# Optimization experiments

Measured on AMD Instinct MI355X. Metric: run time of the kernel, lower is better.

The kernel has to match this reference:

```python
import jax, jax.numpy as jnp
import numpy as np

D_MODEL = 1024
N_HEAD = 16
HEAD_DIM = D_MODEL // N_HEAD


def setup_inputs() -> dict:
    key = jax.random.key(0)
    k1, k2, k3 = jax.random.split(key, 3)
    x = jax.random.normal(k1, (2, 2048, D_MODEL), dtype=jnp.float32)
    w_qkv = jax.random.normal(k2, (D_MODEL, 3 * D_MODEL), dtype=jnp.float32) * (1.0 / np.sqrt(D_MODEL))
    w_proj = jax.random.normal(k3, (D_MODEL, D_MODEL), dtype=jnp.float32) * (1.0 / np.sqrt(D_MODEL))
    return {"x": x, "w_qkv": w_qkv, "w_proj": w_proj}


def reference(x, w_qkv, w_proj):
    bs, sl, dm = x.shape
    qkv = x @ w_qkv                                   # [B,S,3*D]
    qkv = qkv.reshape(bs, sl, 3, N_HEAD, HEAD_DIM)
    q, k, v = qkv[:, :, 0], qkv[:, :, 1], qkv[:, :, 2]  # [B,S,H,d]
    q = q.transpose(0, 2, 1, 3)                        # [B,H,S,d]
    k = k.transpose(0, 2, 1, 3)
    v = v.transpose(0, 2, 1, 3)
    sc = 1.0 / np.sqrt(HEAD_DIM).astype(np.float32)
    attn = jnp.einsum('bhqd,bhkd->bhqk', q, k) * sc    # [B,H,S,S]
    causal = jnp.tril(jnp.ones((sl, sl), dtype=bool))  # True = keep
    attn = jnp.where(causal, attn, -jnp.inf)
    w = jax.nn.softmax(attn, axis=-1)                  # [B,H,S,S] (dropout p=0)
    o = jnp.einsum('bhqk,bhkd->bhqd', w, v)            # [B,H,S,d]
    out = o.transpose(0, 2, 1, 3).reshape(bs, sl, dm)
    out = out @ w_proj
    return (out, w)
```

## Files before the change

kernel.cpp:

```cpp
#include <hip/hip_runtime.h>

typedef _Float16 half8 __attribute__((ext_vector_type(8)));
typedef _Float16 half4 __attribute__((ext_vector_type(4)));
typedef float f32x4 __attribute__((ext_vector_type(4)));

__device__ __forceinline__ void gl2lds16(const _Float16* g, _Float16* l) {
  __builtin_amdgcn_global_load_lds((const __attribute__((address_space(1))) void*)g,
                                   (__attribute__((address_space(3))) void*)l, 16, 0, 0);
}

__device__ __forceinline__ void nt_store4(float* p, f32x4 v) {
  __builtin_nontemporal_store(v, (f32x4*)p);
}

__global__ __launch_bounds__(256) void cvt_kernel(const float* __restrict__ in,
                                                  _Float16* __restrict__ out, int n) {
  int i = (blockIdx.x * 256 + threadIdx.x) * 8;
  if (i >= n) return;
  float4 a = *(const float4*)(in + i);
  float4 b = *(const float4*)(in + i + 4);
  half8 o;
  o[0] = (_Float16)a.x; o[1] = (_Float16)a.y; o[2] = (_Float16)a.z; o[3] = (_Float16)a.w;
  o[4] = (_Float16)b.x; o[5] = (_Float16)b.y; o[6] = (_Float16)b.z; o[7] = (_Float16)b.w;
  *(half8*)(out + i) = o;
}

__global__ __launch_bounds__(256) void cvtT_kernel(const float* __restrict__ in,
                                                   _Float16* __restrict__ out,
                                                   int K, int N) {
  __shared__ float Ts[64][65];
  const int k0 = blockIdx.y * 64, n0 = blockIdx.x * 64;
  const int t = threadIdx.x;
  const int r = t >> 4, c = (t & 15) * 4;
#pragma unroll
  for (int i = 0; i < 4; i++) {
    float4 v = *(const float4*)(in + (size_t)(k0 + r + i * 16) * N + n0 + c);
    Ts[r + i * 16][c] = v.x; Ts[r + i * 16][c + 1] = v.y;
    Ts[r + i * 16][c + 2] = v.z; Ts[r + i * 16][c + 3] = v.w;
  }
  __syncthreads();
  const int nl = t >> 2, kq = (t & 3) * 16;
  half8 o0, o1;
#pragma unroll
  for (int j = 0; j < 8; j++) {
    o0[j] = (_Float16)Ts[kq + j][nl];
    o1[j] = (_Float16)Ts[kq + 8 + j][nl];
  }
  *(half8*)(out + (size_t)(n0 + nl) * K + k0 + kq) = o0;
  *(half8*)(out + (size_t)(n0 + nl) * K + k0 + kq + 8) = o1;
}

__global__ __launch_bounds__(256) void vtrans_kernel(const _Float16* __restrict__ v,
                                                     _Float16* __restrict__ vt) {
  __shared__ _Float16 Ht[64][72];
  const int s0 = blockIdx.x * 64;
  const _Float16* vb = v + (size_t)blockIdx.y * 131072;
  _Float16* vtb = vt + (size_t)blockIdx.y * 131072;
  const int t = threadIdx.x;
  const int sl = t >> 3, dq = (t & 7) * 8;
  *(half8*)&Ht[sl][dq] = *(const half8*)(vb + (s0 + sl) * 64 + dq);
  *(half8*)&Ht[sl + 32][dq] = *(const half8*)(vb + (s0 + sl + 32) * 64 + dq);
  __syncthreads();
  const int dl = t >> 2, sq = (t & 3) * 16;
  half8 o0, o1;
#pragma unroll
  for (int j = 0; j < 8; j++) {
    o0[j] = Ht[sq + j][dl];
    o1[j] = Ht[sq + 8 + j][dl];
  }
  *(half8*)(vtb + (size_t)dl * 2048 + s0 + sq) = o0;
  *(half8*)(vtb + (size_t)dl * 2048 + s0 + sq + 8) = o1;
}

template <int MODE, int BN>
__global__ __launch_bounds__(256) void gemm16(const _Float16* __restrict__ A,
                                              const _Float16* __restrict__ B,
                                              float* __restrict__ Cf,
                                              _Float16* __restrict__ Ch,
                                              int M, int N, int K) {
  constexpr int MI = (BN == 128) ? 4 : 2;
  __shared__ __align__(16) _Float16 As[128 * 32];
  __shared__ __align__(16) _Float16 Bs[BN * 32];
  const int tid = threadIdx.x;
  const int lane = tid & 63;
  const int wid = tid >> 6;
  const int quad = lane >> 4;
  const int l16 = lane & 15;
  const int mbase = (BN == 128) ? (wid >> 1) * 64 : wid * 32;
  const int nbase = (BN == 128) ? (wid & 1) * 64 : 0;
  const int m0 = blockIdx.y * 128;
  const int n0 = blockIdx.x * BN;

  f32x4 acc[MI][4];
  const f32x4 fz = {0.f, 0.f, 0.f, 0.f};
#pragma unroll
  for (int i = 0; i < MI; i++)
#pragma unroll
    for (int j = 0; j < 4; j++) acc[i][j] = fz;

  const int srow = tid >> 2;
  const int kq = (tid & 3) * 8;

  for (int kt = 0; kt < K; kt += 32) {
    gl2lds16(A + (size_t)(m0 + srow) * K + kt + kq, &As[tid * 8]);
    gl2lds16(A + (size_t)(m0 + 64 + srow) * K + kt + kq, &As[2048 + tid * 8]);
    gl2lds16(B + (size_t)(n0 + srow) * K + kt + kq, &Bs[tid * 8]);
    if (BN == 128)
      gl2lds16(B + (size_t)(n0 + 64 + srow) * K + kt + kq, &Bs[2048 + tid * 8]);
    __syncthreads();
    half8 af[MI], bf[4];
#pragma unroll
    for (int mi = 0; mi < MI; mi++)
      af[mi] = *(const half8*)&As[(mbase + mi * 16 + l16) * 32 + quad * 8];
#pragma unroll
    for (int ni = 0; ni < 4; ni++)
      bf[ni] = *(const half8*)&Bs[(nbase + ni * 16 + l16) * 32 + quad * 8];
#pragma unroll
    for (int mi = 0; mi < MI; mi++)
#pragma unroll
      for (int ni = 0; ni < 4; ni++)
        acc[mi][ni] = __builtin_amdgcn_mfma_f32_16x16x32_f16(af[mi], bf[ni], acc[mi][ni], 0, 0, 0);
    __syncthreads();
  }

#pragma unroll
  for (int mi = 0; mi < MI; mi++)
#pragma unroll
    for (int ni = 0; ni < 4; ni++)
#pragma unroll
      for (int r = 0; r < 4; r++) {
        int row = m0 + mbase + mi * 16 + quad * 4 + r;
        int col = n0 + nbase + ni * 16 + l16;
        float v = acc[mi][ni][r];
        if (MODE == 0) {
          Cf[(size_t)row * N + col] = v;
        } else {
          int which = col >> 10, h = (col >> 6) & 15, d = col & 63;
          int b = row >> 11, s = row & 2047;
          Ch[((((size_t)(which * 2 + b) * 16 + h) * 2048) + s) * 64 + d] = (_Float16)v;
        }
      }
}

__global__ __launch_bounds__(256) void attn_kernel(const _Float16* __restrict__ qkv,
                                                   const _Float16* __restrict__ vt,
                                                   float* __restrict__ w_out,
                                                   _Float16* __restrict__ o_buf) {
  const int qt = 31 - blockIdx.x;
  const int bh = blockIdx.y;
  const int tid = threadIdx.x;
  const int lane = tid & 63;
  const int wid = tid >> 6;
  const int quad = lane >> 4;
  const int l16 = lane & 15;

  const _Float16* qp = qkv + (size_t)bh * 131072;
  const _Float16* kp = qp + 4194304;
  const _Float16* vtb = vt + (size_t)bh * 131072;

  __shared__ __align__(16) _Float16 Ks[2][4096];
  __shared__ __align__(16) _Float16 Vs[2][4096];
  __shared__ __align__(16) _Float16 Ps[64][72];

  const int qrow = qt * 64 + wid * 16 + l16;
  const half8 qa0 = *(const half8*)(qp + qrow * 64 + quad * 8);
  const half8 qa1 = *(const half8*)(qp + qrow * 64 + 32 + quad * 8);

  const int srow = tid >> 2;
  const int blk8 = (tid & 3) * 8;
  const float sc = 0.125f;
  const f32x4 fz = {0.f, 0.f, 0.f, 0.f};
  const int lrow0 = wid * 16 + quad * 4;

  float* wbase = w_out + (size_t)bh * 4194304 + (size_t)qt * 131072;

  {
    const int rr = tid >> 4, cc = (tid & 15) * 4;
    for (int kt = qt + 1; kt < 32; kt++) {
      float* wz = wbase + (size_t)kt * 64 + cc;
#pragma unroll
      for (int p = 0; p < 4; p++)
        nt_store4(wz + (size_t)(p * 16 + rr) * 2048, fz);
    }
  }

  float lsum[4] = {0.f, 0.f, 0.f, 0.f};

  int cur = 0;
  gl2lds16(kp + (size_t)srow * 64 + blk8, &Ks[0][tid * 8]);
  gl2lds16(kp + (size_t)srow * 64 + 32 + blk8, &Ks[0][2048 + tid * 8]);
  __syncthreads();
  for (int kt = 0; kt <= qt; kt++) {
    if (kt < qt) {
      gl2lds16(kp + (size_t)((kt + 1) * 64 + srow) * 64 + blk8, &Ks[cur ^ 1][tid * 8]);
      gl2lds16(kp + (size_t)((kt + 1) * 64 + srow) * 64 + 32 + blk8, &Ks[cur ^ 1][2048 + tid * 8]);
    }
    f32x4 sacc[4];
#pragma unroll
    for (int ni = 0; ni < 4; ni++) {
      half8 kb0 = *(const half8*)&Ks[cur][(ni * 16 + l16) * 32 + quad * 8];
      half8 kb1 = *(const half8*)&Ks[cur][2048 + (ni * 16 + l16) * 32 + quad * 8];
      f32x4 s = fz;
      s = __builtin_amdgcn_mfma_f32_16x16x32_f16(qa0, kb0, s, 0, 0, 0);
      s = __builtin_amdgcn_mfma_f32_16x16x32_f16(qa1, kb1, s, 0, 0, 0);
      sacc[ni] = s;
    }
    if (kt < qt) {
#pragma unroll
      for (int ni = 0; ni < 4; ni++)
#pragma unroll
        for (int r = 0; r < 4; r++) lsum[r] += __expf(sacc[ni][r] * sc);
    } else {
#pragma unroll
      for (int ni = 0; ni < 4; ni++)
#pragma unroll
        for (int r = 0; r < 4; r++) {
          if (ni * 16 + l16 <= lrow0 + r) lsum[r] += __expf(sacc[ni][r] * sc);
        }
    }
    __syncthreads();
    cur ^= 1;
  }
  float invl[4];
#pragma unroll
  for (int r = 0; r < 4; r++) {
    float s = lsum[r];
    s += __shfl_xor(s, 1); s += __shfl_xor(s, 2);
    s += __shfl_xor(s, 4); s += __shfl_xor(s, 8);
    invl[r] = 1.0f / s;
  }

  f32x4 oacc[4];
#pragma unroll
  for (int di = 0; di < 4; di++) oacc[di] = fz;

  cur = 0;
  gl2lds16(kp + (size_t)srow * 64 + blk8, &Ks[0][tid * 8]);
  gl2lds16(kp + (size_t)srow * 64 + 32 + blk8, &Ks[0][2048 + tid * 8]);
  gl2lds16(vtb + (size_t)srow * 2048 + blk8, &Vs[0][tid * 8]);
  gl2lds16(vtb + (size_t)srow * 2048 + 32 + blk8, &Vs[0][2048 + tid * 8]);
  __syncthreads();
  for (int kt = 0; kt <= qt; kt++) {
    if (kt < qt) {
      const int kn = kt + 1;
      gl2lds16(kp + (size_t)(kn * 64 + srow) * 64 + blk8, &Ks[cur ^ 1][tid * 8]);
      gl2lds16(kp + (size_t)(kn * 64 + srow) * 64 + 32 + blk8, &Ks[cur ^ 1][2048 + tid * 8]);
      gl2lds16(vtb + (size_t)srow * 2048 + kn * 64 + blk8, &Vs[cur ^ 1][tid * 8]);
      gl2lds16(vtb + (size_t)srow * 2048 + kn * 64 + 32 + blk8, &Vs[cur ^ 1][2048 + tid * 8]);
    }
    f32x4 sacc[4];
#pragma unroll
    for (int ni = 0; ni < 4; ni++) {
      half8 kb0 = *(const half8*)&Ks[cur][(ni * 16 + l16) * 32 + quad * 8];
      half8 kb1 = *(const half8*)&Ks[cur][2048 + (ni * 16 + l16) * 32 + quad * 8];
      f32x4 s = fz;
      s = __builtin_amdgcn_mfma_f32_16x16x32_f16(qa0, kb0, s, 0, 0, 0);
      s = __builtin_amdgcn_mfma_f32_16x16x32_f16(qa1, kb1, s, 0, 0, 0);
      sacc[ni] = s;
    }
#pragma unroll
    for (int ni = 0; ni < 4; ni++)
#pragma unroll
      for (int r = 0; r < 4; r++) {
        int lrw = lrow0 + r;
        int col = ni * 16 + l16;
        float p = __expf(sacc[ni][r] * sc) * invl[r];
        if (kt == qt && col > lrw) p = 0.0f;
        Ps[lrw][col] = (_Float16)p;
      }
#pragma unroll
    for (int kk = 0; kk < 2; kk++) {
      half8 pa = *(const half8*)&Ps[wid * 16 + l16][kk * 32 + quad * 8];
#pragma unroll
      for (int di = 0; di < 4; di++) {
        half8 vb = *(const half8*)&Vs[cur][kk * 2048 + (di * 16 + l16) * 32 + quad * 8];
        oacc[di] = __builtin_amdgcn_mfma_f32_16x16x32_f16(pa, vb, oacc[di], 0, 0, 0);
      }
    }
    {
      const int erow = lane >> 2;
      const int ec = (lane & 3) * 4;
      const _Float16* prow = &Ps[wid * 16 + erow][0];
      float* wrow = wbase + (size_t)(wid * 16 + erow) * 2048 + kt * 64;
#pragma unroll
      for (int j = 0; j < 4; j++) {
        half4 h = *(const half4*)(prow + j * 16 + ec);
        f32x4 o;
        o[0] = (float)h[0]; o[1] = (float)h[1]; o[2] = (float)h[2]; o[3] = (float)h[3];
        nt_store4(wrow + j * 16 + ec, o);
      }
    }
    __syncthreads();
    cur ^= 1;
  }

  const int b = bh >> 4, h = bh & 15;
#pragma unroll
  for (int di = 0; di < 4; di++)
#pragma unroll
    for (int r = 0; r < 4; r++) {
      int s = qt * 64 + lrow0 + r;
      int d = di * 16 + l16;
      o_buf[((size_t)(b * 2048 + s) * 16 + h) * 64 + d] = (_Float16)oacc[di][r];
    }
}

extern "C" void kernel_launch(void* const* d_in, const int* in_sizes, int n_in,
                              void* d_out, int out_size, void* d_ws, size_t ws_size,
                              hipStream_t stream) {
  const float* x = (const float*)d_in[0];
  const float* w_qkv = (const float*)d_in[1];
  const float* w_proj = (const float*)d_in[2];
  float* out = (float*)d_out;
  float* w_attn = out + (size_t)4194304;

  char* ws = (char*)d_ws;
  _Float16* x16 = (_Float16*)ws;
  _Float16* wqkvT = (_Float16*)(ws + (size_t)(8 << 20));
  _Float16* wprojT = (_Float16*)(ws + (size_t)(14 << 20));
  _Float16* qkvb = (_Float16*)(ws + (size_t)(16 << 20));
  _Float16* vT = (_Float16*)(ws + (size_t)(40 << 20));
  _Float16* ob = (_Float16*)(ws + (size_t)(48 << 20));

  cvt_kernel<<<2048, 256, 0, stream>>>(x, x16, 4194304);
  cvtT_kernel<<<dim3(48, 16), 256, 0, stream>>>(w_qkv, wqkvT, 1024, 3072);
  cvtT_kernel<<<dim3(16, 16), 256, 0, stream>>>(w_proj, wprojT, 1024, 1024);

  gemm16<1, 128><<<dim3(24, 32), 256, 0, stream>>>(x16, wqkvT, nullptr, qkvb, 4096, 3072, 1024);
  vtrans_kernel<<<dim3(32, 32), 256, 0, stream>>>(qkvb + (size_t)2 * 4194304, vT);
  attn_kernel<<<dim3(32, 32), 256, 0, stream>>>(qkvb, vT, w_attn, ob);
  gemm16<0, 64><<<dim3(16, 32), 256, 0, stream>>>(ob, wprojT, out, nullptr, 4096, 1024, 1024);
}
```

Before: 699.1 us.

## Load K/V fragments straight from global memory, drop LDS staging and barriers

The attention kernel stops staging K and V tiles through double-buffered LDS with global_load_lds and block-wide barriers. Each wave now reads its MFMA operand fragments directly from global memory and relies on the caches for reuse across waves. The softmax scale is folded into Q at the QKV GEMM epilogue, and s_setprio is raised around the MFMA sections. The aim is to remove barrier stalls and LDS traffic, at the cost of more global and L2 load requests and exposed load latency with no explicit prefetch.

```diff
diff --git a/kernel.cpp b/kernel.cpp
--- a/kernel.cpp
+++ b/kernel.cpp
@@ -137,6 +137,7 @@
         } else {
           int which = col >> 10, h = (col >> 6) & 15, d = col & 63;
           int b = row >> 11, s = row & 2047;
+          if (which == 0) v *= 0.125f;
           Ch[((((size_t)(which * 2 + b) * 16 + h) * 2048) + s) * 64 + d] = (_Float16)v;
         }
       }
@@ -158,17 +159,12 @@
   const _Float16* kp = qp + 4194304;
   const _Float16* vtb = vt + (size_t)bh * 131072;
 
-  __shared__ __align__(16) _Float16 Ks[2][4096];
-  __shared__ __align__(16) _Float16 Vs[2][4096];
   __shared__ __align__(16) _Float16 Ps[64][72];
 
   const int qrow = qt * 64 + wid * 16 + l16;
   const half8 qa0 = *(const half8*)(qp + qrow * 64 + quad * 8);
   const half8 qa1 = *(const half8*)(qp + qrow * 64 + 32 + quad * 8);
 
-  const int srow = tid >> 2;
-  const int blk8 = (tid & 3) * 8;
-  const float sc = 0.125f;
   const f32x4 fz = {0.f, 0.f, 0.f, 0.f};
   const int lrow0 = wid * 16 + quad * 4;
 
@@ -186,40 +182,33 @@
 
   float lsum[4] = {0.f, 0.f, 0.f, 0.f};
 
-  int cur = 0;
-  gl2lds16(kp + (size_t)srow * 64 + blk8, &Ks[0][tid * 8]);
-  gl2lds16(kp + (size_t)srow * 64 + 32 + blk8, &Ks[0][2048 + tid * 8]);
-  __syncthreads();
   for (int kt = 0; kt <= qt; kt++) {
-    if (kt < qt) {
-      gl2lds16(kp + (size_t)((kt + 1) * 64 + srow) * 64 + blk8, &Ks[cur ^ 1][tid * 8]);
-      gl2lds16(kp + (size_t)((kt + 1) * 64 + srow) * 64 + 32 + blk8, &Ks[cur ^ 1][2048 + tid * 8]);
-    }
+    const _Float16* kb = kp + (size_t)kt * 4096;
     f32x4 sacc[4];
+    __builtin_amdgcn_s_setprio(1);
 #pragma unroll
     for (int ni = 0; ni < 4; ni++) {
-      half8 kb0 = *(const half8*)&Ks[cur][(ni * 16 + l16) * 32 + quad * 8];
-      half8 kb1 = *(const half8*)&Ks[cur][2048 + (ni * 16 + l16) * 32 + quad * 8];
+      half8 kb0 = *(const half8*)(kb + (ni * 16 + l16) * 64 + quad * 8);
+      half8 kb1 = *(const half8*)(kb + (ni * 16 + l16) * 64 + 32 + quad * 8);
       f32x4 s = fz;
       s = __builtin_amdgcn_mfma_f32_16x16x32_f16(qa0, kb0, s, 0, 0, 0);
       s = __builtin_amdgcn_mfma_f32_16x16x32_f16(qa1, kb1, s, 0, 0, 0);
       sacc[ni] = s;
     }
+    __builtin_amdgcn_s_setprio(0);
     if (kt < qt) {
 #pragma unroll
       for (int ni = 0; ni < 4; ni++)
 #pragma unroll
-        for (int r = 0; r < 4; r++) lsum[r] += __expf(sacc[ni][r] * sc);
+        for (int r = 0; r < 4; r++) lsum[r] += __expf(sacc[ni][r]);
     } else {
 #pragma unroll
       for (int ni = 0; ni < 4; ni++)
 #pragma unroll
         for (int r = 0; r < 4; r++) {
-          if (ni * 16 + l16 <= lrow0 + r) lsum[r] += __expf(sacc[ni][r] * sc);
+          if (ni * 16 + l16 <= lrow0 + r) lsum[r] += __expf(sacc[ni][r]);
         }
     }
-    __syncthreads();
-    cur ^= 1;
   }
   float invl[4];
 #pragma unroll
@@ -234,49 +223,41 @@
 #pragma unroll
   for (int di = 0; di < 4; di++) oacc[di] = fz;
 
-  cur = 0;
-  gl2lds16(kp + (size_t)srow * 64 + blk8, &Ks[0][tid * 8]);
-  gl2lds16(kp + (size_t)srow * 64 + 32 + blk8, &Ks[0][2048 + tid * 8]);
-  gl2lds16(vtb + (size_t)srow * 2048 + blk8, &Vs[0][tid * 8]);
-  gl2lds16(vtb + (size_t)srow * 2048 + 32 + blk8, &Vs[0][2048 + tid * 8]);
-  __syncthreads();
   for (int kt = 0; kt <= qt; kt++) {
-    if (kt < qt) {
-      const int kn = kt + 1;
-      gl2lds16(kp + (size_t)(kn * 64 + srow) * 64 + blk8, &Ks[cur ^ 1][tid * 8]);
-      gl2lds16(kp + (size_t)(kn * 64 + srow) * 64 + 32 + blk8, &Ks[cur ^ 1][2048 + tid * 8]);
-      gl2lds16(vtb + (size_t)srow * 2048 + kn * 64 + blk8, &Vs[cur ^ 1][tid * 8]);
-      gl2lds16(vtb + (size_t)srow * 2048 + kn * 64 + 32 + blk8, &Vs[cur ^ 1][2048 + tid * 8]);
-    }
+    const _Float16* kb = kp + (size_t)kt * 4096;
     f32x4 sacc[4];
+    __builtin_amdgcn_s_setprio(1);
 #pragma unroll
     for (int ni = 0; ni < 4; ni++) {
-      half8 kb0 = *(const half8*)&Ks[cur][(ni * 16 + l16) * 32 + quad * 8];
-      half8 kb1 = *(const half8*)&Ks[cur][2048 + (ni * 16 + l16) * 32 + quad * 8];
+      half8 kb0 = *(const half8*)(kb + (ni * 16 + l16) * 64 + quad * 8);
+      half8 kb1 = *(const half8*)(kb + (ni * 16 + l16) * 64 + 32 + quad * 8);
       f32x4 s = fz;
       s = __builtin_amdgcn_mfma_f32_16x16x32_f16(qa0, kb0, s, 0, 0, 0);
       s = __builtin_amdgcn_mfma_f32_16x16x32_f16(qa1, kb1, s, 0, 0, 0);
       sacc[ni] = s;
     }
+    __builtin_amdgcn_s_setprio(0);
 #pragma unroll
     for (int ni = 0; ni < 4; ni++)
 #pragma unroll
       for (int r = 0; r < 4; r++) {
         int lrw = lrow0 + r;
         int col = ni * 16 + l16;
-        float p = __expf(sacc[ni][r] * sc) * invl[r];
+        float p = __expf(sacc[ni][r]) * invl[r];
         if (kt == qt && col > lrw) p = 0.0f;
         Ps[lrw][col] = (_Float16)p;
       }
+    __builtin_amdgcn_s_setprio(1);
 #pragma unroll
     for (int kk = 0; kk < 2; kk++) {
       half8 pa = *(const half8*)&Ps[wid * 16 + l16][kk * 32 + quad * 8];
 #pragma unroll
       for (int di = 0; di < 4; di++) {
-        half8 vb = *(const half8*)&Vs[cur][kk * 2048 + (di * 16 + l16) * 32 + quad * 8];
+        half8 vb = *(const half8*)(vtb + (size_t)(di * 16 + l16) * 2048 + kt * 64 + kk * 32 + quad * 8);
         oacc[di] = __builtin_amdgcn_mfma_f32_16x16x32_f16(pa, vb, oacc[di], 0, 0, 0);
       }
     }
+    __builtin_amdgcn_s_setprio(0);
     {
       const int erow = lane >> 2;
       const int ec = (lane & 3) * 4;
@@ -290,8 +271,6 @@
         nt_store4(wrow + j * 16 + ec, o);
       }
     }
-    __syncthreads();
-    cur ^= 1;
   }
 
   const int b = bh >> 4, h = bh & 15;
```

Result: slower. 889.4 us (+27.2%).

## Fold softmax scale into Q and load V fragments directly from global

Applied to the files above, without the earlier changes.

The QKV GEMM epilogue now multiplies Q by 1/sqrt(d) before storing it, so the attention kernel no longer scales each score before the exponential. The V tile is no longer staged through double-buffered shared memory with global-to-LDS copies. Each wave instead loads its V MFMA fragments straight from global memory into registers at the start of each key tile. The barrier is moved to sit before the W store. This cuts LDS traffic and footprint and drops one multiply per score, but each wave now loads V redundantly, and that load latency is hidden only behind the QK MFMAs.

```diff
diff --git a/kernel.cpp b/kernel.cpp
--- a/kernel.cpp
+++ b/kernel.cpp
@@ -137,6 +137,7 @@
         } else {
           int which = col >> 10, h = (col >> 6) & 15, d = col & 63;
           int b = row >> 11, s = row & 2047;
+          if (which == 0) v *= 0.125f;
           Ch[((((size_t)(which * 2 + b) * 16 + h) * 2048) + s) * 64 + d] = (_Float16)v;
         }
       }
@@ -159,7 +160,6 @@
   const _Float16* vtb = vt + (size_t)bh * 131072;
 
   __shared__ __align__(16) _Float16 Ks[2][4096];
-  __shared__ __align__(16) _Float16 Vs[2][4096];
   __shared__ __align__(16) _Float16 Ps[64][72];
 
   const int qrow = qt * 64 + wid * 16 + l16;
@@ -168,7 +168,6 @@
 
   const int srow = tid >> 2;
   const int blk8 = (tid & 3) * 8;
-  const float sc = 0.125f;
   const f32x4 fz = {0.f, 0.f, 0.f, 0.f};
   const int lrow0 = wid * 16 + quad * 4;
 
@@ -209,13 +208,13 @@
 #pragma unroll
       for (int ni = 0; ni < 4; ni++)
 #pragma unroll
-        for (int r = 0; r < 4; r++) lsum[r] += __expf(sacc[ni][r] * sc);
+        for (int r = 0; r < 4; r++) lsum[r] += __expf(sacc[ni][r]);
     } else {
 #pragma unroll
       for (int ni = 0; ni < 4; ni++)
 #pragma unroll
         for (int r = 0; r < 4; r++) {
-          if (ni * 16 + l16 <= lrow0 + r) lsum[r] += __expf(sacc[ni][r] * sc);
+          if (ni * 16 + l16 <= lrow0 + r) lsum[r] += __expf(sacc[ni][r]);
         }
     }
     __syncthreads();
@@ -237,16 +236,17 @@
   cur = 0;
   gl2lds16(kp + (size_t)srow * 64 + blk8, &Ks[0][tid * 8]);
   gl2lds16(kp + (size_t)srow * 64 + 32 + blk8, &Ks[0][2048 + tid * 8]);
-  gl2lds16(vtb + (size_t)srow * 2048 + blk8, &Vs[0][tid * 8]);
-  gl2lds16(vtb + (size_t)srow * 2048 + 32 + blk8, &Vs[0][2048 + tid * 8]);
   __syncthreads();
   for (int kt = 0; kt <= qt; kt++) {
+    half8 vr[2][4];
+#pragma unroll
+    for (int kk = 0; kk < 2; kk++)
+#pragma unroll
+      for (int di = 0; di < 4; di++)
+        vr[kk][di] = *(const half8*)(vtb + (size_t)(di * 16 + l16) * 2048 + kt * 64 + kk * 32 + quad * 8);
     if (kt < qt) {
-      const int kn = kt + 1;
-      gl2lds16(kp + (size_t)(kn * 64 + srow) * 64 + blk8, &Ks[cur ^ 1][tid * 8]);
-      gl2lds16(kp + (size_t)(kn * 64 + srow) * 64 + 32 + blk8, &Ks[cur ^ 1][2048 + tid * 8]);
-      gl2lds16(vtb + (size_t)srow * 2048 + kn * 64 + blk8, &Vs[cur ^ 1][tid * 8]);
-      gl2lds16(vtb + (size_t)srow * 2048 + kn * 64 + 32 + blk8, &Vs[cur ^ 1][2048 + tid * 8]);
+      gl2lds16(kp + (size_t)((kt + 1) * 64 + srow) * 64 + blk8, &Ks[cur ^ 1][tid * 8]);
+      gl2lds16(kp + (size_t)((kt + 1) * 64 + srow) * 64 + 32 + blk8, &Ks[cur ^ 1][2048 + tid * 8]);
     }
     f32x4 sacc[4];
 #pragma unroll
@@ -264,7 +264,7 @@
       for (int r = 0; r < 4; r++) {
         int lrw = lrow0 + r;
         int col = ni * 16 + l16;
-        float p = __expf(sacc[ni][r] * sc) * invl[r];
+        float p = __expf(sacc[ni][r]) * invl[r];
         if (kt == qt && col > lrw) p = 0.0f;
         Ps[lrw][col] = (_Float16)p;
       }
@@ -272,11 +272,10 @@
     for (int kk = 0; kk < 2; kk++) {
       half8 pa = *(const half8*)&Ps[wid * 16 + l16][kk * 32 + quad * 8];
 #pragma unroll
-      for (int di = 0; di < 4; di++) {
-        half8 vb = *(const half8*)&Vs[cur][kk * 2048 + (di * 16 + l16) * 32 + quad * 8];
-        oacc[di] = __builtin_amdgcn_mfma_f32_16x16x32_f16(pa, vb, oacc[di], 0, 0, 0);
-      }
-    }
+      for (int di = 0; di < 4; di++)
+        oacc[di] = __builtin_amdgcn_mfma_f32_16x16x32_f16(pa, vr[kk][di], oacc[di], 0, 0, 0);
+    }
+    __syncthreads();
     {
       const int erow = lane >> 2;
       const int ec = (lane & 3) * 4;
@@ -290,7 +289,6 @@
         nt_store4(wrow + j * 16 + ec, o);
       }
     }
-    __syncthreads();
     cur ^= 1;
   }
 
```

Measured after the change: 735.9 us. +5.3%, slower.
